# Kernel tuning notes

Measured on AMD Instinct MI355X. Metric: run time of the kernel, lower is better.

Reference implementation:

```python
import jax, jax.numpy as jnp
import numpy as np

SIZE_DICT = 1024
DIM_DICT = 256
BETA = 0.001


def setup_inputs() -> dict:
    key = jax.random.key(0)
    k1, k2 = jax.random.split(key)
    z = jax.random.normal(k1, (64, 1024, DIM_DICT), dtype=jnp.float32)
    codebook = jax.random.normal(k2, (SIZE_DICT, DIM_DICT), dtype=jnp.float32)
    return {"z": z, "codebook": codebook, "flg_train": 1}


def reference(z, codebook, flg_train):
    zf = z.reshape(-1, DIM_DICT)  # [N, D]
    # squared euclidean distances: ||z||^2 + ||c||^2 - 2 z c^T  -> [N, K]
    d = (jnp.sum(zf ** 2, axis=1, keepdims=True)
         + jnp.sum(codebook ** 2, axis=1)
         - 2.0 * jnp.matmul(zf, codebook.T))
    idx = jnp.argmin(d, axis=1)  # [N]
    # one-hot @ codebook == gather
    z_q = codebook[idx].reshape(z.shape)
    if flg_train:
        loss = (jnp.mean((jax.lax.stop_gradient(z_q) - z) ** 2)
                + BETA * jnp.mean((z_q - jax.lax.stop_gradient(z)) ** 2))
    else:
        loss = jnp.float32(0.0)
    # straight-through estimator
    z_q = z + jax.lax.stop_gradient(z_q - z)
    # perplexity from codebook usage histogram (== mean of one-hot rows)
    n = zf.shape[0]
    counts = jax.ops.segment_sum(jnp.ones((n,), jnp.float32), idx,
                                 num_segments=SIZE_DICT)
    e_mean = counts / n
    perplexity = jnp.exp(-jnp.sum(e_mean * jnp.log(e_mean + 1e-10)))
    return (z_q, loss, perplexity)
```

## Files before the change

kernel.cpp:

```cpp
#include <hip/hip_runtime.h>


#define N_ROWS 65536
#define DIM    256
#define K_CODES 1024
#define BETA   0.001f

#define BM      128
#define NBLOCKS (N_ROWS / BM)
#define NTHREADS 512
#define CHUNK_BYTES 65536
#define NCHUNK  16

#define LO_SCALE 2048.0f
#define LO_INV   (1.0f / 2048.0f)

#define WS_BESTS_OFF 16384
#define WS_CBIMG_OFF 278528
#define WS_NEED (WS_CBIMG_OFF + NCHUNK * CHUNK_BYTES)

typedef _Float16 f16x8 __attribute__((ext_vector_type(8)));
typedef float f32x16 __attribute__((ext_vector_type(16)));


__global__ void cnorm_kernel(const float* __restrict__ cb, float* __restrict__ cnorm) {
    int k = blockIdx.x * blockDim.x + threadIdx.x;
    if (k >= K_CODES) return;
    const float4* row = (const float4*)(cb + (size_t)k * DIM);
    float s = 0.f;
#pragma unroll
    for (int j = 0; j < DIM / 4; ++j) {
        float4 v = row[j];
        s = fmaf(v.x, v.x, s);
        s = fmaf(v.y, v.y, s);
        s = fmaf(v.z, v.z, s);
        s = fmaf(v.w, v.w, s);
    }
    cnorm[k] = s;
}

__global__ void cb_prep(const float* __restrict__ cb, char* __restrict__ img) {
    int idx = blockIdx.x * blockDim.x + threadIdx.x;
    int c   = idx >> 5;
    int g32 = idx & 31;
    const float4* src = (const float4*)(cb + (size_t)c * DIM + g32 * 8);
    float4 v0 = src[0], v1 = src[1];
    float vv[8] = {v0.x, v0.y, v0.z, v0.w, v1.x, v1.y, v1.z, v1.w};
    f16x8 hi, lo;
#pragma unroll
    for (int j = 0; j < 8; ++j) {
        _Float16 h = (_Float16)vv[j];
        hi[j] = h;
        lo[j] = (_Float16)((vv[j] - (float)h) * LO_SCALE);
    }
    int kh = g32 >> 4;
    int gl = g32 & 15;
    int cl = c & 63;
    int gp = gl ^ (cl & 7);
    int unit = (c >> 6) * 2 + kh;
    size_t off = (size_t)unit * 32768 + (size_t)cl * 256 + (size_t)gp * 16;
    *(f16x8*)(img + off) = hi;
    *(f16x8*)(img + off + 16384) = lo;
}


__device__ inline void stage_chunk(const char* img, int c, char* ldsbase, int tid) {
#pragma unroll
    for (int i = 0; i < 8; ++i) {
        __builtin_amdgcn_global_load_lds(
            (const __attribute__((address_space(1))) unsigned int*)
                (img + (size_t)c * CHUNK_BYTES + i * 8192 + tid * 16),
            (__attribute__((address_space(3))) unsigned int*)
                (ldsbase + i * 8192 + tid * 16),
            16, 0, 0);
    }
}

#define LOADB(KS, BH, BL)                                                            \
    {                                                                                \
        const _Float16* p = bbase + ((KS) >> 3) * 16384 +                            \
                            (((((KS) & 7) * 2) + lh) ^ csw) * 8;                     \
        BH = *(const f16x8*)(p);                                                     \
        BL = *(const f16x8*)(p + 8192);                                              \
    }

#define MF(KS, BH, BL)                                                               \
    {                                                                                \
        f16x8 ah = zh[KS], al = zl[KS];                                              \
        acc_hh = __builtin_amdgcn_mfma_f32_32x32x16_f16(ah, BH, acc_hh, 0, 0, 0);    \
        acc_x  = __builtin_amdgcn_mfma_f32_32x32x16_f16(ah, BL, acc_x, 0, 0, 0);     \
        acc_x  = __builtin_amdgcn_mfma_f32_32x32x16_f16(al, BH, acc_x, 0, 0, 0);     \
    }

#define COMPUTE_CHUNK(BUF)                                                           \
    {                                                                                \
        const _Float16* bbase = csb + (BUF) * 32768 + crow * 128;                    \
        f16x8 bhA, blA, bhB, blB;                                                    \
        LOADB(0, bhA, blA)                                                           \
        LOADB(1, bhB, blB)                                                           \
        _Pragma("unroll")                                                            \
        for (int ks = 0; ks < 16; ks += 2) {                                         \
            MF(ks, bhA, blA)                                                         \
            if (ks + 2 < 16) LOADB(ks + 2, bhA, blA)                                 \
            MF(ks + 1, bhB, blB)                                                     \
            if (ks + 3 < 16) LOADB(ks + 3, bhB, blB)                                 \
        }                                                                            \
    }

__global__ __launch_bounds__(NTHREADS, 2)
void vq_main_mfma(const float* __restrict__ z, const char* __restrict__ img,
                  const float* __restrict__ cnorm, int* __restrict__ bests_g,
                  int* __restrict__ counts, float* __restrict__ ploss) {
    __shared__ _Float16 csb[2 * 32768];
    __shared__ float bs2[BM][2];
    __shared__ int   bc2[BM][2];
    __shared__ float znorm_lds[BM];
    __shared__ float red[NTHREADS];

    const int tid  = threadIdx.x;
    const int lane = tid & 63;
    const int w    = tid >> 6;
    const int wr   = w >> 1;
    const int wc   = w & 1;
    const int l31  = lane & 31;
    const int lh   = lane >> 5;
    const int r0   = blockIdx.x * BM;

    stage_chunk(img, 0, (char*)csb, tid);

    const int zrow = wr * 32 + l31;
    f16x8 zh[16], zl[16];
    {
        const float* zr = z + (size_t)(r0 + zrow) * DIM;
        float zn = 0.f;
#pragma unroll
        for (int gi = 0; gi < 16; ++gi) {
            int g = gi * 2 + lh;
            float4 v0 = *(const float4*)(zr + g * 8);
            float4 v1 = *(const float4*)(zr + g * 8 + 4);
            float vv[8] = {v0.x, v0.y, v0.z, v0.w, v1.x, v1.y, v1.z, v1.w};
            f16x8 hi, lo;
#pragma unroll
            for (int j = 0; j < 8; ++j) {
                _Float16 h = (_Float16)vv[j];
                hi[j] = h;
                lo[j] = (_Float16)((vv[j] - (float)h) * LO_SCALE);
                zn = fmaf(vv[j], vv[j], zn);
            }
            zh[gi] = hi;
            zl[gi] = lo;
        }
        zn += __shfl_xor(zn, 32, 64);
        if (wc == 0 && lh == 0) znorm_lds[zrow] = zn;
    }

    f32x16 acc_hh, acc_x;
#pragma unroll
    for (int e = 0; e < 16; ++e) { acc_hh[e] = 0.f; acc_x[e] = 0.f; }
    float best_s[16];
    int   best_c[16];
#pragma unroll
    for (int e = 0; e < 16; ++e) { best_s[e] = 3.4e38f; best_c[e] = 0; }

    const int crow = wc * 32 + l31;
    const int csw  = crow & 7;

#pragma unroll 1
    for (int c = 0; c < NCHUNK; ++c) {
        const int b = c & 1;
        asm volatile("" ::: "memory");
        __builtin_amdgcn_s_barrier();
        asm volatile("" ::: "memory");
        if (c + 1 < NCHUNK) {
            stage_chunk(img, c + 1, (char*)csb + (b ^ 1) * CHUNK_BYTES, tid);
            asm volatile("s_waitcnt vmcnt(8)" ::: "memory");
        } else {
            asm volatile("s_waitcnt vmcnt(0)" ::: "memory");
        }
        __builtin_amdgcn_s_barrier();
        asm volatile("" ::: "memory");

        __builtin_amdgcn_s_setprio(1);
        COMPUTE_CHUNK(b)
        __builtin_amdgcn_s_setprio(0);

        {
            int col = c * 64 + crow;
            float cn = cnorm[col];
#pragma unroll
            for (int rg = 0; rg < 16; ++rg) {
                float s = fmaf(-2.0f, fmaf(acc_x[rg], LO_INV, acc_hh[rg]), cn);
                bool take = s < best_s[rg];
                best_s[rg] = take ? s : best_s[rg];
                best_c[rg] = take ? col : best_c[rg];
            }
#pragma unroll
            for (int e = 0; e < 16; ++e) { acc_hh[e] = 0.f; acc_x[e] = 0.f; }
        }
    }

#pragma unroll
    for (int rg = 0; rg < 16; ++rg) {
        float bsv = best_s[rg];
        int   bcv = best_c[rg];
#pragma unroll
        for (int s = 1; s < 32; s <<= 1) {
            float os = __shfl_xor(bsv, s, 64);
            int   oc = __shfl_xor(bcv, s, 64);
            bool take = (os < bsv) || (os == bsv && oc < bcv);
            bsv = take ? os : bsv;
            bcv = take ? oc : bcv;
        }
        best_s[rg] = bsv;
        best_c[rg] = bcv;
    }
    if (l31 == 0) {
#pragma unroll
        for (int rg = 0; rg < 16; ++rg) {
            int rl = (rg & 3) + 8 * (rg >> 2) + 4 * lh;
            bs2[wr * 32 + rl][wc] = best_s[rg];
            bc2[wr * 32 + rl][wc] = best_c[rg];
        }
    }
    __syncthreads();

    float lsum = 0.f;
    if (tid < BM) {
        float s0 = bs2[tid][0], s1 = bs2[tid][1];
        int   c0 = bc2[tid][0], c1 = bc2[tid][1];
        bool t1 = (s1 < s0) || (s1 == s0 && c1 < c0);
        int   bc = t1 ? c1 : c0;
        float bs = t1 ? s1 : s0;
        bests_g[r0 + tid] = bc;
        atomicAdd(&counts[bc], 1);
        lsum = bs + znorm_lds[tid];
    }
    red[tid] = lsum;
    __syncthreads();
    for (int s = NTHREADS / 2; s > 0; s >>= 1) {
        if (tid < s) red[tid] += red[tid + s];
        __syncthreads();
    }
    if (tid == 0) ploss[blockIdx.x] = red[0];
}


__global__ __launch_bounds__(256)
void vq_gather(const float4* __restrict__ cb4, const int* __restrict__ bests,
               float4* __restrict__ out4) {
    int gid = blockIdx.x * blockDim.x + threadIdx.x;
    int row = gid >> 6;
    int q   = gid & 63;
    out4[gid] = cb4[(size_t)bests[row] * 64 + q];
}


#define FBM     32
#define FCHUNK  512
#define FDSTAGE 16
#define FCS_PAD 20
#define FNBLOCKS (N_ROWS / FBM)

__global__ __launch_bounds__(256, 2)
void vq_main_fp32(const float* __restrict__ z, const float* __restrict__ cb,
                  const float* __restrict__ cnorm, float* __restrict__ out,
                  int* __restrict__ counts, float* __restrict__ ploss) {
    __shared__ float zs[FBM][DIM];
    __shared__ float cs[FCHUNK][FCS_PAD];
    __shared__ int   bests[FBM];
    __shared__ float red[256];

    const int tid = threadIdx.x;
    const int tx  = tid & 63;
    const int ty  = tid >> 6;
    const int r0  = blockIdx.x * FBM;

    {
        const float4* zg  = (const float4*)(z + (size_t)r0 * DIM);
        float4*       zsv = (float4*)&zs[0][0];
#pragma unroll
        for (int j = 0; j < (FBM * DIM / 4) / 256; ++j)
            zsv[tid + 256 * j] = zg[tid + 256 * j];
    }

    unsigned long long best[8];
#pragma unroll
    for (int i = 0; i < 8; ++i) best[i] = ~0ull;

    for (int cb0 = 0; cb0 < K_CODES; cb0 += FCHUNK) {
        float acc[8][8];
#pragma unroll
        for (int i = 0; i < 8; ++i)
#pragma unroll
            for (int m = 0; m < 8; ++m) acc[i][m] = 0.f;

        for (int sd = 0; sd < DIM / FDSTAGE; ++sd) {
            __syncthreads();
#pragma unroll
            for (int j = 0; j < 8; ++j) {
                int f4i = tid + 256 * j;
                int c   = f4i >> 2;
                int qq  = f4i & 3;
                float4 v = *(const float4*)(cb + (size_t)(cb0 + c) * DIM + sd * FDSTAGE + qq * 4);
                *(float4*)&cs[c][qq * 4] = v;
            }
            __syncthreads();

#pragma unroll
            for (int dd4 = 0; dd4 < FDSTAGE / 4; ++dd4) {
                float4 zv[8], cv[8];
#pragma unroll
                for (int i = 0; i < 8; ++i)
                    zv[i] = *(const float4*)&zs[ty * 8 + i][sd * FDSTAGE + dd4 * 4];
#pragma unroll
                for (int m = 0; m < 8; ++m)
                    cv[m] = *(const float4*)&cs[tx + 64 * m][dd4 * 4];
#pragma unroll
                for (int i = 0; i < 8; ++i)
#pragma unroll
                    for (int m = 0; m < 8; ++m) {
                        float a = acc[i][m];
                        a = fmaf(zv[i].x, cv[m].x, a);
                        a = fmaf(zv[i].y, cv[m].y, a);
                        a = fmaf(zv[i].z, cv[m].z, a);
                        a = fmaf(zv[i].w, cv[m].w, a);
                        acc[i][m] = a;
                    }
            }
        }

#pragma unroll
        for (int m = 0; m < 8; ++m) {
            int   c  = cb0 + tx + 64 * m;
            float cn = cnorm[c];
#pragma unroll
            for (int i = 0; i < 8; ++i) {
                float s = fmaf(-2.f, acc[i][m], cn);
                unsigned u = __float_as_uint(s);
                u = (u & 0x80000000u) ? ~u : (u | 0x80000000u);
                unsigned long long key = ((unsigned long long)u << 32) | (unsigned)c;
                best[i] = key < best[i] ? key : best[i];
            }
        }
    }

#pragma unroll
    for (int i = 0; i < 8; ++i) {
        unsigned long long b = best[i];
#pragma unroll
        for (int s = 1; s < 64; s <<= 1) {
            unsigned long long o = __shfl_xor(b, s, 64);
            b = o < b ? o : b;
        }
        best[i] = b;
    }
    if (tx == 0)
#pragma unroll
        for (int i = 0; i < 8; ++i)
            bests[ty * 8 + i] = (int)(best[i] & 0xFFFFFFFFu);
    __syncthreads();

    const int r  = tid >> 3;
    const int lq = tid & 7;
    const int bidx = bests[r];
    const float4* crow = (const float4*)(cb + (size_t)bidx * DIM);
    const float4* zrow = (const float4*)&zs[r][0];
    float4*       orow = (float4*)(out + (size_t)(r0 + r) * DIM);
    float lsum = 0.f;
#pragma unroll
    for (int j = 0; j < 8; ++j) {
        int qg = lq + j * 8;
        float4 c4 = crow[qg];
        float4 z4 = zrow[qg];
        float4 o;
        float dx = c4.x - z4.x; o.x = z4.x + dx; lsum = fmaf(dx, dx, lsum);
        float dy = c4.y - z4.y; o.y = z4.y + dy; lsum = fmaf(dy, dy, lsum);
        float dz = c4.z - z4.z; o.z = z4.z + dz; lsum = fmaf(dz, dz, lsum);
        float dw = c4.w - z4.w; o.w = z4.w + dw; lsum = fmaf(dw, dw, lsum);
        orow[qg] = o;
    }
    if (tid < FBM) atomicAdd(&counts[bests[tid]], 1);

    red[tid] = lsum;
    __syncthreads();
    for (int s = 128; s > 0; s >>= 1) {
        if (tid < s) red[tid] += red[tid + s];
        __syncthreads();
    }
    if (tid == 0) ploss[blockIdx.x] = red[0];
}


__global__ void vq_final(const float* __restrict__ ploss, const int* __restrict__ counts,
                         const int* __restrict__ flg, float* __restrict__ out2, int np) {
    __shared__ float red[1024];
    const int t = threadIdx.x;

    float l = 0.f;
    for (int i = t; i < np; i += 1024) l += ploss[i];
    red[t] = l;
    __syncthreads();
    for (int s = 512; s > 0; s >>= 1) {
        if (t < s) red[t] += red[t + s];
        __syncthreads();
    }
    if (t == 0) {
        float loss = (red[0] / (float)((size_t)N_ROWS * DIM)) * (1.0f + BETA);
        if (flg[0] == 0) loss = 0.f;
        out2[0] = loss;
    }
    __syncthreads();

    float e = (float)counts[t] / (float)N_ROWS;
    red[t] = e * logf(e + 1e-10f);
    __syncthreads();
    for (int s = 512; s > 0; s >>= 1) {
        if (t < s) red[t] += red[t + s];
        __syncthreads();
    }
    if (t == 0) out2[1] = expf(-red[0]);
}

extern "C" void kernel_launch(void* const* d_in, const int* in_sizes, int n_in,
                              void* d_out, int out_size, void* d_ws, size_t ws_size,
                              hipStream_t stream) {
    const float* z   = (const float*)d_in[0];
    const float* cb  = (const float*)d_in[1];
    const int*   flg = (const int*)d_in[2];
    float* out = (float*)d_out;
    float* ws  = (float*)d_ws;

    float* cnorm  = ws;
    int*   counts = (int*)((char*)d_ws + 4096);
    float* ploss  = (float*)((char*)d_ws + 8192);
    int*   bests  = (int*)((char*)d_ws + WS_BESTS_OFF);
    char*  cbimg  = (char*)d_ws + WS_CBIMG_OFF;

    hipMemsetAsync(counts, 0, K_CODES * sizeof(int), stream);
    cnorm_kernel<<<K_CODES / 256, 256, 0, stream>>>(cb, cnorm);

    if (ws_size >= (size_t)WS_NEED) {
        cb_prep<<<128, 256, 0, stream>>>(cb, cbimg);
        vq_main_mfma<<<NBLOCKS, NTHREADS, 0, stream>>>(z, cbimg, cnorm, bests, counts, ploss);
        vq_gather<<<(N_ROWS * 64) / 256, 256, 0, stream>>>((const float4*)cb, bests, (float4*)out);
        vq_final<<<1, 1024, 0, stream>>>(ploss, counts, flg, out + (size_t)N_ROWS * DIM, NBLOCKS);
    } else {
        vq_main_fp32<<<FNBLOCKS, 256, 0, stream>>>(z, cb, cnorm, out, counts, ploss);
        vq_final<<<1, 1024, 0, stream>>>(ploss, counts, flg, out + (size_t)N_ROWS * DIM, FNBLOCKS);
    }
}
```

Baseline: 177.1 us.

## Split MFMA accumulators into independent chains and transpose codebook LDS layout

Replaces the two serially dependent MFMA accumulators with six independent ones (two hi*hi, four cross terms) so consecutive MFMAs no longer wait on each other, then sums them in the epilogue. It also changes the codebook image layout from a per-code XOR-swizzled row to a k-group-major layout, where each code's 16-byte slice sits at a stride of 16 bytes across codes. The LDS read addressing is adjusted to match. This costs extra accumulator registers (96 more VGPR/AGPR), which may pressure occupancy at two blocks per CU. It also changes LDS bank access patterns and slightly reorders the floating-point summation.

```diff
diff --git a/kernel.cpp b/kernel.cpp
--- a/kernel.cpp
+++ b/kernel.cpp
@@ -56,9 +56,8 @@
     int kh = g32 >> 4;
     int gl = g32 & 15;
     int cl = c & 63;
-    int gp = gl ^ (cl & 7);
     int unit = (c >> 6) * 2 + kh;
-    size_t off = (size_t)unit * 32768 + (size_t)cl * 256 + (size_t)gp * 16;
+    size_t off = (size_t)unit * 32768 + (size_t)gl * 1024 + (size_t)cl * 16;
     *(f16x8*)(img + off) = hi;
     *(f16x8*)(img + off + 16384) = lo;
 }
@@ -78,31 +77,30 @@
 
 #define LOADB(KS, BH, BL)                                                            \
     {                                                                                \
-        const _Float16* p = bbase + ((KS) >> 3) * 16384 +                            \
-                            (((((KS) & 7) * 2) + lh) ^ csw) * 8;                     \
+        const _Float16* p = bbase + ((KS) >> 3) * 16384 + (((KS) & 7) * 2 + lh) * 512;\
         BH = *(const f16x8*)(p);                                                     \
         BL = *(const f16x8*)(p + 8192);                                              \
     }
 
-#define MF(KS, BH, BL)                                                               \
+#define MF(KS, BH, BL, HH, X1, X2)                                                   \
     {                                                                                \
         f16x8 ah = zh[KS], al = zl[KS];                                              \
-        acc_hh = __builtin_amdgcn_mfma_f32_32x32x16_f16(ah, BH, acc_hh, 0, 0, 0);    \
-        acc_x  = __builtin_amdgcn_mfma_f32_32x32x16_f16(ah, BL, acc_x, 0, 0, 0);     \
-        acc_x  = __builtin_amdgcn_mfma_f32_32x32x16_f16(al, BH, acc_x, 0, 0, 0);     \
+        HH = __builtin_amdgcn_mfma_f32_32x32x16_f16(ah, BH, HH, 0, 0, 0);            \
+        X1 = __builtin_amdgcn_mfma_f32_32x32x16_f16(ah, BL, X1, 0, 0, 0);            \
+        X2 = __builtin_amdgcn_mfma_f32_32x32x16_f16(al, BH, X2, 0, 0, 0);            \
     }
 
 #define COMPUTE_CHUNK(BUF)                                                           \
     {                                                                                \
-        const _Float16* bbase = csb + (BUF) * 32768 + crow * 128;                    \
+        const _Float16* bbase = csb + (BUF) * 32768 + crow * 8;                      \
         f16x8 bhA, blA, bhB, blB;                                                    \
         LOADB(0, bhA, blA)                                                           \
         LOADB(1, bhB, blB)                                                           \
         _Pragma("unroll")                                                            \
         for (int ks = 0; ks < 16; ks += 2) {                                         \
-            MF(ks, bhA, blA)                                                         \
+            MF(ks, bhA, blA, acc_hhe, acc_xa, acc_xb)                                \
             if (ks + 2 < 16) LOADB(ks + 2, bhA, blA)                                 \
-            MF(ks + 1, bhB, blB)                                                     \
+            MF(ks + 1, bhB, blB, acc_hho, acc_xc, acc_xd)                            \
             if (ks + 3 < 16) LOADB(ks + 3, bhB, blB)                                 \
         }                                                                            \
     }
@@ -154,16 +152,19 @@
         if (wc == 0 && lh == 0) znorm_lds[zrow] = zn;
     }
 
-    f32x16 acc_hh, acc_x;
-#pragma unroll
-    for (int e = 0; e < 16; ++e) { acc_hh[e] = 0.f; acc_x[e] = 0.f; }
+    f32x16 acc_hhe, acc_hho, acc_xa, acc_xb, acc_xc, acc_xd;
+#pragma unroll
+    for (int e = 0; e < 16; ++e) {
+        acc_hhe[e] = 0.f; acc_hho[e] = 0.f;
+        acc_xa[e] = 0.f;  acc_xb[e] = 0.f;
+        acc_xc[e] = 0.f;  acc_xd[e] = 0.f;
+    }
     float best_s[16];
     int   best_c[16];
 #pragma unroll
     for (int e = 0; e < 16; ++e) { best_s[e] = 3.4e38f; best_c[e] = 0; }
 
     const int crow = wc * 32 + l31;
-    const int csw  = crow & 7;
 
 #pragma unroll 1
     for (int c = 0; c < NCHUNK; ++c) {
@@ -189,13 +190,19 @@
             float cn = cnorm[col];
 #pragma unroll
             for (int rg = 0; rg < 16; ++rg) {
-                float s = fmaf(-2.0f, fmaf(acc_x[rg], LO_INV, acc_hh[rg]), cn);
+                float xsum = (acc_xa[rg] + acc_xb[rg]) + (acc_xc[rg] + acc_xd[rg]);
+                float dot  = fmaf(xsum, LO_INV, acc_hhe[rg] + acc_hho[rg]);
+                float s = fmaf(-2.0f, dot, cn);
                 bool take = s < best_s[rg];
                 best_s[rg] = take ? s : best_s[rg];
                 best_c[rg] = take ? col : best_c[rg];
             }
 #pragma unroll
-            for (int e = 0; e < 16; ++e) { acc_hh[e] = 0.f; acc_x[e] = 0.f; }
+            for (int e = 0; e < 16; ++e) {
+                acc_hhe[e] = 0.f; acc_hho[e] = 0.f;
+                acc_xa[e] = 0.f;  acc_xb[e] = 0.f;
+                acc_xc[e] = 0.f;  acc_xd[e] = 0.f;
+            }
         }
     }
 
```

New measurement: 200.8 us. 13.4% more time.
